# Kernel optimization log

Measured on AMD Instinct MI355X. Metric: run time of the kernel, lower is better.

Reference implementation:

```python
import jax, jax.numpy as jnp
import numpy as np

N = 100000
E = 1600000
F_IN = 512
HEADS = 8
C1 = 8          # per-head channels layer 1
C2 = 16         # num_classes, layer 2 (heads=1)
NEG_SLOPE = 0.2


def gat_conv(x, W, att_src, att_dst, bias, edge_index, heads, ch):
    """PyG-style GATConv (eval mode, add_self_loops=True, concat).
    x: [N, Fin], W: [Fin, heads*ch], att_*: [heads, ch], bias: [heads*ch]."""
    n = x.shape[0]
    loop = jnp.arange(n, dtype=edge_index.dtype)
    src = jnp.concatenate([edge_index[0], loop])   # [E+N]
    dst = jnp.concatenate([edge_index[1], loop])

    h = (x @ W).reshape(n, heads, ch)                       # [N, H, C]
    a_src = jnp.einsum('nhc,hc->nh', h, att_src)            # [N, H]
    a_dst = jnp.einsum('nhc,hc->nh', h, att_dst)

    e = a_src[src] + a_dst[dst]                             # [E+N, H]
    e = jax.nn.leaky_relu(e, NEG_SLOPE)
    # segment softmax over destination nodes
    m = jax.ops.segment_max(e, dst, num_segments=n)         # [N, H]
    ex = jnp.exp(e - m[dst])
    denom = jax.ops.segment_sum(ex, dst, num_segments=n)    # [N, H]
    alpha = ex / (denom[dst] + 1e-16)                       # [E+N, H]

    msg = h[src] * alpha[..., None]                         # [E+N, H, C]
    out = jax.ops.segment_sum(msg, dst, num_segments=n)     # [N, H, C]
    return out.reshape(n, heads * ch) + bias


def setup_inputs() -> dict:
    key = jax.random.key(0)
    ks = jax.random.split(key, 10)
    glorot = lambda k, shape: jax.random.normal(k, shape, jnp.float32) * np.sqrt(2.0 / (shape[0] + shape[-1]))
    return {
        'x': jax.random.normal(ks[0], (N, F_IN), jnp.float32),
        'edge_index': jax.random.randint(ks[1], (2, E), 0, N, jnp.int64),
        'W1': glorot(ks[2], (F_IN, HEADS * C1)),
        'att_src1': glorot(ks[3], (HEADS, C1)),
        'att_dst1': glorot(ks[4], (HEADS, C1)),
        'b1': jnp.zeros((HEADS * C1,), jnp.float32),
        'W2': glorot(ks[5], (HEADS * C1, C2)),
        'att_src2': glorot(ks[6], (1, C2)),
        'att_dst2': glorot(ks[7], (1, C2)),
        'b2': jnp.zeros((C2,), jnp.float32),
    }


def reference(x, edge_index, W1, att_src1, att_dst1, b1, W2, att_src2, att_dst2, b2):
    # eval mode: all F.dropout / internal attention dropout are identity
    h = gat_conv(x, W1, att_src1, att_dst1, b1, edge_index, HEADS, C1)   # [N, 64]
    h = jax.nn.elu(h)
    h = gat_conv(h, W2, att_src2, att_dst2, b2, edge_index, 1, C2)       # [N, C2]
    return jax.nn.log_softmax(h, axis=1)
```

## Files before the change

### kernel.cpp

```cpp
#include <hip/hip_runtime.h>
#include <hip/hip_bf16.h>

#define NEG_SLOPE 0.2f

typedef __attribute__((ext_vector_type(8))) short  bf16x8;
typedef __attribute__((ext_vector_type(8))) unsigned short u16x8;
typedef __attribute__((ext_vector_type(4))) unsigned short u16x4;
typedef __attribute__((ext_vector_type(4))) float  f32x4;

static __device__ __forceinline__ ushort f2bf(float f) {
    union { float f; unsigned int u; } c; c.f = f;
    unsigned int r = c.u + 0x7fffu + ((c.u >> 16) & 1u);
    return (ushort)(r >> 16);
}
static __device__ __forceinline__ float bf2f(ushort u) {
    union { unsigned int u; float f; } c; c.u = ((unsigned int)u) << 16;
    return c.f;
}

__global__ __launch_bounds__(256) void prep_w1(const float* __restrict__ W, ushort* __restrict__ W1T)
{
    int idx = blockIdx.x * 256 + threadIdx.x;
    if (idx >= 64 * 512) return;
    int c = idx >> 9, k = idx & 511;
    W1T[idx] = f2bf(W[k * 64 + c]);
}

__global__ __launch_bounds__(512, 4) void gemm1_mfma(
    const float* __restrict__ x, const ushort* __restrict__ W1T,
    const float* __restrict__ att_src, const float* __restrict__ att_dst,
    ushort* __restrict__ h1b, float* __restrict__ asrc, float* __restrict__ adst, int n)
{
    __shared__ ushort Bs[64][520];
    const int t    = threadIdx.x;
    const int lane = t & 63;
    const int wv   = t >> 6;
    const int rb   = blockIdx.x * 128;
    const int m    = lane & 15;
    const int kg   = lane >> 4;

    #pragma unroll
    for (int i = 0; i < 8; ++i) {
        int chunk = t + i * 512;
        int c  = chunk >> 6;
        int ko = (chunk & 63) * 8;
        *(u16x8*)&Bs[c][ko] = *(const u16x8*)(W1T + c * 512 + ko);
    }

    const int arow  = rb + wv * 16 + m;
    const int arowc = min(arow, n - 1);
    const float* xp = x + (size_t)arowc * 512 + kg * 8;

    f32x4 acc[4] = {};
    __syncthreads();

    float4 lo0 = *(const float4*)(xp);
    float4 hi0 = *(const float4*)(xp + 4);
    float4 lo1 = *(const float4*)(xp + 32);
    float4 hi1 = *(const float4*)(xp + 36);
    #pragma unroll
    for (int k32 = 0; k32 < 16; ++k32) {
        float4 nlo = {}, nhi = {};
        if (k32 < 14) {
            nlo = *(const float4*)(xp + (k32 + 2) * 32);
            nhi = *(const float4*)(xp + (k32 + 2) * 32 + 4);
        }
        u16x8 a;
        a[0] = f2bf(lo0.x); a[1] = f2bf(lo0.y); a[2] = f2bf(lo0.z); a[3] = f2bf(lo0.w);
        a[4] = f2bf(hi0.x); a[5] = f2bf(hi0.y); a[6] = f2bf(hi0.z); a[7] = f2bf(hi0.w);
        bf16x8 af = *(bf16x8*)&a;
        #pragma unroll
        for (int t4 = 0; t4 < 4; ++t4) {
            bf16x8 bfr = *(const bf16x8*)&Bs[t4 * 16 + m][k32 * 32 + kg * 8];
            acc[t4] = __builtin_amdgcn_mfma_f32_16x16x32_bf16(af, bfr, acc[t4], 0, 0, 0);
        }
        lo0 = lo1; hi0 = hi1; lo1 = nlo; hi1 = nhi;
    }

    #pragma unroll
    for (int t4 = 0; t4 < 4; ++t4) {
        const float as_w = att_src[t4 * 16 + m];
        const float ad_w = att_dst[t4 * 16 + m];
        #pragma unroll
        for (int i = 0; i < 4; ++i) {
            int gr = rb + wv * 16 + kg * 4 + i;
            float v = acc[t4][i];
            float ps = v * as_w, pd = v * ad_w;
            ps += __shfl_xor(ps, 1); pd += __shfl_xor(pd, 1);
            ps += __shfl_xor(ps, 2); pd += __shfl_xor(pd, 2);
            ps += __shfl_xor(ps, 4); pd += __shfl_xor(pd, 4);
            if (gr < n) {
                h1b[(size_t)gr * 64 + t4 * 16 + m] = f2bf(v);
                if ((m & 7) == 0) {
                    int h = t4 * 2 + (m >> 3);
                    asrc[gr * 8 + h] = ps;
                    adst[gr * 8 + h] = pd;
                }
            }
        }
    }
}

__global__ __launch_bounds__(256) void hist_k(
    const int* __restrict__ ei, int* __restrict__ cnt, int* __restrict__ slot, int E)
{
    int t = blockIdx.x * blockDim.x + threadIdx.x;
    if (t < E) slot[t] = atomicAdd(&cnt[ei[E + t]], 1);
}

#define SCAN_B 256
#define SCAN_T 256

__global__ __launch_bounds__(SCAN_T) void scan_a(const int* __restrict__ cnt, int* __restrict__ bsum, int n)
{
    __shared__ int sh[SCAN_T];
    const int tid = threadIdx.x;
    const int per = (n + SCAN_B * SCAN_T - 1) / (SCAN_B * SCAN_T);
    const int lo = (blockIdx.x * SCAN_T + tid) * per;
    const int hi = min(n, lo + per);
    int s = 0;
    for (int i = lo; i < hi; ++i) s += cnt[i];
    sh[tid] = s;
    __syncthreads();
    #pragma unroll
    for (int o = SCAN_T / 2; o; o >>= 1) {
        if (tid < o) sh[tid] += sh[tid + o];
        __syncthreads();
    }
    if (tid == 0) bsum[blockIdx.x] = sh[0];
}

__global__ __launch_bounds__(SCAN_T) void scan_b(
    const int* __restrict__ cnt, const int* __restrict__ bsum,
    int* __restrict__ rowptr, int n, int E)
{
    __shared__ int sb[SCAN_B];
    __shared__ int sh[SCAN_T];
    const int tid = threadIdx.x;
    sb[tid] = bsum[tid];
    __syncthreads();
    #pragma unroll
    for (int o = 1; o < SCAN_B; o <<= 1) {
        int v = (tid >= o) ? sb[tid - o] : 0;
        __syncthreads();
        sb[tid] += v;
        __syncthreads();
    }
    const int boff = (blockIdx.x == 0) ? 0 : sb[blockIdx.x - 1];

    const int per = (n + SCAN_B * SCAN_T - 1) / (SCAN_B * SCAN_T);
    const int lo = (blockIdx.x * SCAN_T + tid) * per;
    const int hi = min(n, lo + per);
    int s = 0;
    for (int i = lo; i < hi; ++i) s += cnt[i];
    sh[tid] = s;
    __syncthreads();
    #pragma unroll
    for (int o = 1; o < SCAN_T; o <<= 1) {
        int v = (tid >= o) ? sh[tid - o] : 0;
        __syncthreads();
        sh[tid] += v;
        __syncthreads();
    }
    int excl = boff + ((tid == 0) ? 0 : sh[tid - 1]);
    for (int i = lo; i < hi; ++i) { rowptr[i] = excl; excl += cnt[i]; }
    if (blockIdx.x == 0 && tid == 0) rowptr[n] = E;
}

__global__ __launch_bounds__(256) void scatter_k(
    const int* __restrict__ ei, const int* __restrict__ rowptr,
    const int* __restrict__ slot, int* __restrict__ ssrc, int E)
{
    int t = blockIdx.x * blockDim.x + threadIdx.x;
    if (t >= E) return;
    int d = ei[E + t];
    ssrc[rowptr[d] + slot[t]] = ei[t];
}

__global__ __launch_bounds__(256) void agg1_k(
    const int* __restrict__ rowptr, const int* __restrict__ ssrc,
    const float* __restrict__ asrc1, const float* __restrict__ adst1,
    const ushort* __restrict__ h1b, const float* __restrict__ b1,
    const float* __restrict__ W2, const float* __restrict__ att_src2, const float* __restrict__ att_dst2,
    ushort* __restrict__ h2b, float* __restrict__ asrc2, float* __restrict__ adst2, int n)
{
    __shared__ float Ws2[64 * 17];
    __shared__ float sv[4][64];
    const int t = threadIdx.x;
    #pragma unroll
    for (int k = 0; k < 4; ++k) {
        int idx = t + k * 256;
        Ws2[(idx >> 4) * 17 + (idx & 15)] = W2[idx];
    }
    __syncthreads();

    const int wv = t >> 6;
    const int j  = t & 63;
    const int g  = j >> 3;
    const int h  = j & 7;
    const int node = blockIdx.x * 4 + wv;
    const bool active = node < n;

    if (active) {
        const int d = node;
        const int start = rowptr[d], end = rowptr[d + 1];
        const float adsth = adst1[d * 8 + h];
        float acc0[8] = {}, acc1[8] = {};
        float dsum0 = 0.f, dsum1 = 0.f;
        for (int base = start - 1; base < end; base += 16) {
            int i0 = base + g;
            int i1 = i0 + 8;
            if (i0 < end) {
                int s = (i0 < start) ? d : ssrc[i0];
                float e = asrc1[s * 8 + h] + adsth;
                e = e > 0.f ? e : NEG_SLOPE * e;
                float ex = __expf(e);
                dsum0 += ex;
                u16x8 hv = *(const u16x8*)(h1b + (size_t)s * 64 + h * 8);
                #pragma unroll
                for (int c = 0; c < 8; ++c) acc0[c] += ex * bf2f(hv[c]);
            }
            if (i1 < end) {
                int s = ssrc[i1];
                float e = asrc1[s * 8 + h] + adsth;
                e = e > 0.f ? e : NEG_SLOPE * e;
                float ex = __expf(e);
                dsum1 += ex;
                u16x8 hv = *(const u16x8*)(h1b + (size_t)s * 64 + h * 8);
                #pragma unroll
                for (int c = 0; c < 8; ++c) acc1[c] += ex * bf2f(hv[c]);
            }
        }
        float dsum = dsum0 + dsum1;
        float acc[8];
        #pragma unroll
        for (int c = 0; c < 8; ++c) acc[c] = acc0[c] + acc1[c];
        #pragma unroll
        for (int o = 8; o < 64; o <<= 1) {
            dsum += __shfl_xor(dsum, o);
            #pragma unroll
            for (int c = 0; c < 8; ++c) acc[c] += __shfl_xor(acc[c], o);
        }
        if (g == 0) {
            float den = dsum + 1e-16f;
            #pragma unroll
            for (int c = 0; c < 8; ++c) {
                float v = acc[c] / den + b1[h * 8 + c];
                v = v > 0.f ? v : (__expf(v) - 1.f);
                sv[wv][h * 8 + c] = v;
            }
        }
    }
    __syncthreads();

    if (active) {
        const int c = j & 15, q = j >> 4;
        float p = 0.f;
        #pragma unroll
        for (int r = 0; r < 16; ++r)
            p += sv[wv][q * 16 + r] * Ws2[(q * 16 + r) * 17 + c];
        p += __shfl_xor(p, 16);
        p += __shfl_xor(p, 32);
        if (j < 16) h2b[(size_t)node * 16 + j] = f2bf(p);
        float as2 = p * att_src2[c];
        float ad2 = p * att_dst2[c];
        #pragma unroll
        for (int o = 1; o < 16; o <<= 1) { as2 += __shfl_xor(as2, o, 16); ad2 += __shfl_xor(ad2, o, 16); }
        if (j == 0) { asrc2[node] = as2; adst2[node] = ad2; }
    }
}

__global__ __launch_bounds__(256) void agg2_k(
    const int* __restrict__ rowptr, const int* __restrict__ ssrc,
    const float* __restrict__ asrc2, const float* __restrict__ adst2,
    const ushort* __restrict__ h2b, const float* __restrict__ b2,
    float* __restrict__ out, int n)
{
    const int t = threadIdx.x;
    const int node = blockIdx.x * 4 + (t >> 6);
    if (node >= n) return;
    const int j = t & 63;
    const int g = j >> 2;
    const int q = j & 3;
    const int d = node;
    const int start = rowptr[d], end = rowptr[d + 1];
    const float adst_d = adst2[d];

    float acc0[4] = {}, acc1[4] = {};
    float dsum0 = 0.f, dsum1 = 0.f;
    for (int base = start - 1; base < end; base += 32) {
        int i0 = base + g;
        int i1 = i0 + 16;
        if (i0 < end) {
            int s = (i0 < start) ? d : ssrc[i0];
            float e = asrc2[s] + adst_d;
            e = e > 0.f ? e : NEG_SLOPE * e;
            float ex = __expf(e);
            dsum0 += ex;
            u16x4 hv = *(const u16x4*)(h2b + (size_t)s * 16 + q * 4);
            #pragma unroll
            for (int c = 0; c < 4; ++c) acc0[c] += ex * bf2f(hv[c]);
        }
        if (i1 < end) {
            int s = ssrc[i1];
            float e = asrc2[s] + adst_d;
            e = e > 0.f ? e : NEG_SLOPE * e;
            float ex = __expf(e);
            dsum1 += ex;
            u16x4 hv = *(const u16x4*)(h2b + (size_t)s * 16 + q * 4);
            #pragma unroll
            for (int c = 0; c < 4; ++c) acc1[c] += ex * bf2f(hv[c]);
        }
    }
    float dsum = dsum0 + dsum1;
    float acc[4];
    #pragma unroll
    for (int c = 0; c < 4; ++c) acc[c] = acc0[c] + acc1[c];
    #pragma unroll
    for (int o = 4; o < 64; o <<= 1) {
        dsum += __shfl_xor(dsum, o);
        #pragma unroll
        for (int c = 0; c < 4; ++c) acc[c] += __shfl_xor(acc[c], o);
    }

    const float den = dsum + 1e-16f;
    float v[4];
    float m = -1e30f;
    #pragma unroll
    for (int c = 0; c < 4; ++c) {
        v[c] = acc[c] / den + b2[q * 4 + c];
        m = fmaxf(m, v[c]);
    }
    m = fmaxf(m, __shfl_xor(m, 1));
    m = fmaxf(m, __shfl_xor(m, 2));
    float s2 = 0.f;
    #pragma unroll
    for (int c = 0; c < 4; ++c) s2 += __expf(v[c] - m);
    s2 += __shfl_xor(s2, 1);
    s2 += __shfl_xor(s2, 2);
    const float lse = m + logf(s2);
    if (j < 4) {
        float4 o4 = make_float4(v[0] - lse, v[1] - lse, v[2] - lse, v[3] - lse);
        *(float4*)(out + (size_t)d * 16 + q * 4) = o4;
    }
}

static inline size_t align_up(size_t v, size_t a) { return (v + a - 1) & ~(a - 1); }

extern "C" void kernel_launch(void* const* d_in, const int* in_sizes, int n_in,
                              void* d_out, int out_size, void* d_ws, size_t ws_size,
                              hipStream_t stream) {
    const float* x        = (const float*)d_in[0];
    const int*   ei       = (const int*)d_in[1];
    const float* W1       = (const float*)d_in[2];
    const float* att_src1 = (const float*)d_in[3];
    const float* att_dst1 = (const float*)d_in[4];
    const float* b1       = (const float*)d_in[5];
    const float* W2       = (const float*)d_in[6];
    const float* att_src2 = (const float*)d_in[7];
    const float* att_dst2 = (const float*)d_in[8];
    const float* b2       = (const float*)d_in[9];
    float* out = (float*)d_out;

    const int n = in_sizes[0] / 512;
    const int E = in_sizes[1] / 2;

    char* base = (char*)d_ws;
    size_t off = 0;
    ushort* h1b   = (ushort*)(base + off); off = align_up(off + (size_t)128 * n, 64);
    ushort* h2b   = (ushort*)(base + off); off = align_up(off + (size_t)32 * n, 64);
    float*  asrc1 = (float*) (base + off); off = align_up(off + (size_t)32 * n, 64);
    float*  adst1 = (float*) (base + off); off = align_up(off + (size_t)32 * n, 64);
    float*  asrc2 = (float*) (base + off); off = align_up(off + (size_t)4 * n, 64);
    float*  adst2 = (float*) (base + off); off = align_up(off + (size_t)4 * n, 64);
    ushort* W1T   = (ushort*)(base + off); off = align_up(off + (size_t)65536, 64);
    int*    rowptr= (int*)   (base + off); off = align_up(off + (size_t)4 * (n + 1), 64);
    int*    cnt   = (int*)   (base + off); off = align_up(off + (size_t)4 * n, 64);
    int*    bsum  = (int*)   (base + off); off = align_up(off + (size_t)1024, 64);
    int*    slot  = (int*)   (base + off); off = align_up(off + (size_t)4 * E, 64);
    int*    ssrc  = (int*)   (base + off);

    hipMemsetAsync(cnt, 0, (size_t)4 * n, stream);

    prep_w1<<<128, 256, 0, stream>>>(W1, W1T);

    hist_k<<<(E + 255) / 256, 256, 0, stream>>>(ei, cnt, slot, E);
    scan_a<<<SCAN_B, SCAN_T, 0, stream>>>(cnt, bsum, n);
    scan_b<<<SCAN_B, SCAN_T, 0, stream>>>(cnt, bsum, rowptr, n, E);
    scatter_k<<<(E + 255) / 256, 256, 0, stream>>>(ei, rowptr, slot, ssrc, E);

    gemm1_mfma<<<(n + 127) / 128, 512, 0, stream>>>(x, W1T, att_src1, att_dst1, h1b, asrc1, adst1, n);

    agg1_k<<<(n + 3) / 4, 256, 0, stream>>>(rowptr, ssrc, asrc1, adst1, h1b, b1,
                                            W2, att_src2, att_dst2, h2b, asrc2, adst2, n);

    agg2_k<<<(n + 3) / 4, 256, 0, stream>>>(rowptr, ssrc, asrc2, adst2, h2b, b2, out, n);
}
```

Baseline: 269.3 us.

## Merge independent kernels via block-range dispatch and deepen x prefetch in GEMM

Combines W1 transpose/convert with the degree histogram into one launch, and the CSR scatter with the layer-1 GEMM into another, picking the role by block index so independent work shares a grid. This removes two kernel launches and lets the scatter and GEMM blocks run concurrently. The GEMM's register prefetch of x is also deepened from two to four k-steps ahead, raising register use. Scatter blocks now carry the GEMM's large static LDS allocation and the 512-thread, 4-wave-per-EU launch bounds, which may lower their occupancy.

```diff
diff --git a/kernel.cpp b/kernel.cpp
--- a/kernel.cpp
+++ b/kernel.cpp
@@ -18,24 +18,101 @@
     return c.f;
 }
 
-__global__ __launch_bounds__(256) void prep_w1(const float* __restrict__ W, ushort* __restrict__ W1T)
-{
-    int idx = blockIdx.x * 256 + threadIdx.x;
-    if (idx >= 64 * 512) return;
-    int c = idx >> 9, k = idx & 511;
-    W1T[idx] = f2bf(W[k * 64 + c]);
-}
-
-__global__ __launch_bounds__(512, 4) void gemm1_mfma(
+__global__ __launch_bounds__(256) void phase1_k(
+    const float* __restrict__ W, ushort* __restrict__ W1T,
+    const int* __restrict__ ei, int* __restrict__ cnt, int* __restrict__ slot, int E)
+{
+    if (blockIdx.x < 128) {
+        int idx = blockIdx.x * 256 + threadIdx.x;
+        int c = idx >> 9, k = idx & 511;
+        W1T[idx] = f2bf(W[k * 64 + c]);
+    } else {
+        int t = (blockIdx.x - 128) * 256 + threadIdx.x;
+        if (t < E) slot[t] = atomicAdd(&cnt[ei[E + t]], 1);
+    }
+}
+
+#define SCAN_B 256
+#define SCAN_T 256
+
+__global__ __launch_bounds__(SCAN_T) void scan_a(const int* __restrict__ cnt, int* __restrict__ bsum, int n)
+{
+    __shared__ int sh[SCAN_T];
+    const int tid = threadIdx.x;
+    const int per = (n + SCAN_B * SCAN_T - 1) / (SCAN_B * SCAN_T);
+    const int lo = (blockIdx.x * SCAN_T + tid) * per;
+    const int hi = min(n, lo + per);
+    int s = 0;
+    for (int i = lo; i < hi; ++i) s += cnt[i];
+    sh[tid] = s;
+    __syncthreads();
+    #pragma unroll
+    for (int o = SCAN_T / 2; o; o >>= 1) {
+        if (tid < o) sh[tid] += sh[tid + o];
+        __syncthreads();
+    }
+    if (tid == 0) bsum[blockIdx.x] = sh[0];
+}
+
+__global__ __launch_bounds__(SCAN_T) void scan_b(
+    const int* __restrict__ cnt, const int* __restrict__ bsum,
+    int* __restrict__ rowptr, int n, int E)
+{
+    __shared__ int sb[SCAN_B];
+    __shared__ int sh[SCAN_T];
+    const int tid = threadIdx.x;
+    sb[tid] = bsum[tid];
+    __syncthreads();
+    #pragma unroll
+    for (int o = 1; o < SCAN_B; o <<= 1) {
+        int v = (tid >= o) ? sb[tid - o] : 0;
+        __syncthreads();
+        sb[tid] += v;
+        __syncthreads();
+    }
+    const int boff = (blockIdx.x == 0) ? 0 : sb[blockIdx.x - 1];
+
+    const int per = (n + SCAN_B * SCAN_T - 1) / (SCAN_B * SCAN_T);
+    const int lo = (blockIdx.x * SCAN_T + tid) * per;
+    const int hi = min(n, lo + per);
+    int s = 0;
+    for (int i = lo; i < hi; ++i) s += cnt[i];
+    sh[tid] = s;
+    __syncthreads();
+    #pragma unroll
+    for (int o = 1; o < SCAN_T; o <<= 1) {
+        int v = (tid >= o) ? sh[tid - o] : 0;
+        __syncthreads();
+        sh[tid] += v;
+        __syncthreads();
+    }
+    int excl = boff + ((tid == 0) ? 0 : sh[tid - 1]);
+    for (int i = lo; i < hi; ++i) { rowptr[i] = excl; excl += cnt[i]; }
+    if (blockIdx.x == 0 && tid == 0) rowptr[n] = E;
+}
+
+__global__ __launch_bounds__(512, 4) void phase4_k(
+    const int* __restrict__ ei, const int* __restrict__ rowptr,
+    const int* __restrict__ slot, int* __restrict__ ssrc, int E, int Gs,
     const float* __restrict__ x, const ushort* __restrict__ W1T,
     const float* __restrict__ att_src, const float* __restrict__ att_dst,
     ushort* __restrict__ h1b, float* __restrict__ asrc, float* __restrict__ adst, int n)
 {
     __shared__ ushort Bs[64][520];
+
+    if ((int)blockIdx.x < Gs) {
+        int t = blockIdx.x * 512 + threadIdx.x;
+        if (t < E) {
+            int d = ei[E + t];
+            ssrc[rowptr[d] + slot[t]] = ei[t];
+        }
+        return;
+    }
+
     const int t    = threadIdx.x;
     const int lane = t & 63;
     const int wv   = t >> 6;
-    const int rb   = blockIdx.x * 128;
+    const int rb   = (blockIdx.x - Gs) * 128;
     const int m    = lane & 15;
     const int kg   = lane >> 4;
 
@@ -54,27 +131,28 @@
     f32x4 acc[4] = {};
     __syncthreads();
 
-    float4 lo0 = *(const float4*)(xp);
-    float4 hi0 = *(const float4*)(xp + 4);
-    float4 lo1 = *(const float4*)(xp + 32);
-    float4 hi1 = *(const float4*)(xp + 36);
+    float4 plo[4], phi[4];
+    #pragma unroll
+    for (int i = 0; i < 4; ++i) {
+        plo[i] = *(const float4*)(xp + i * 32);
+        phi[i] = *(const float4*)(xp + i * 32 + 4);
+    }
     #pragma unroll
     for (int k32 = 0; k32 < 16; ++k32) {
-        float4 nlo = {}, nhi = {};
-        if (k32 < 14) {
-            nlo = *(const float4*)(xp + (k32 + 2) * 32);
-            nhi = *(const float4*)(xp + (k32 + 2) * 32 + 4);
+        float4 lo = plo[k32 & 3], hi = phi[k32 & 3];
+        if (k32 + 4 < 16) {
+            plo[k32 & 3] = *(const float4*)(xp + (k32 + 4) * 32);
+            phi[k32 & 3] = *(const float4*)(xp + (k32 + 4) * 32 + 4);
         }
         u16x8 a;
-        a[0] = f2bf(lo0.x); a[1] = f2bf(lo0.y); a[2] = f2bf(lo0.z); a[3] = f2bf(lo0.w);
-        a[4] = f2bf(hi0.x); a[5] = f2bf(hi0.y); a[6] = f2bf(hi0.z); a[7] = f2bf(hi0.w);
+        a[0] = f2bf(lo.x); a[1] = f2bf(lo.y); a[2] = f2bf(lo.z); a[3] = f2bf(lo.w);
+        a[4] = f2bf(hi.x); a[5] = f2bf(hi.y); a[6] = f2bf(hi.z); a[7] = f2bf(hi.w);
         bf16x8 af = *(bf16x8*)&a;
         #pragma unroll
         for (int t4 = 0; t4 < 4; ++t4) {
             bf16x8 bfr = *(const bf16x8*)&Bs[t4 * 16 + m][k32 * 32 + kg * 8];
             acc[t4] = __builtin_amdgcn_mfma_f32_16x16x32_bf16(af, bfr, acc[t4], 0, 0, 0);
         }
-        lo0 = lo1; hi0 = hi1; lo1 = nlo; hi1 = nhi;
     }
 
     #pragma unroll
@@ -99,82 +177,6 @@
             }
         }
     }
-}
-
-__global__ __launch_bounds__(256) void hist_k(
-    const int* __restrict__ ei, int* __restrict__ cnt, int* __restrict__ slot, int E)
-{
-    int t = blockIdx.x * blockDim.x + threadIdx.x;
-    if (t < E) slot[t] = atomicAdd(&cnt[ei[E + t]], 1);
-}
-
-#define SCAN_B 256
-#define SCAN_T 256
-
-__global__ __launch_bounds__(SCAN_T) void scan_a(const int* __restrict__ cnt, int* __restrict__ bsum, int n)
-{
-    __shared__ int sh[SCAN_T];
-    const int tid = threadIdx.x;
-    const int per = (n + SCAN_B * SCAN_T - 1) / (SCAN_B * SCAN_T);
-    const int lo = (blockIdx.x * SCAN_T + tid) * per;
-    const int hi = min(n, lo + per);
-    int s = 0;
-    for (int i = lo; i < hi; ++i) s += cnt[i];
-    sh[tid] = s;
-    __syncthreads();
-    #pragma unroll
-    for (int o = SCAN_T / 2; o; o >>= 1) {
-        if (tid < o) sh[tid] += sh[tid + o];
-        __syncthreads();
-    }
-    if (tid == 0) bsum[blockIdx.x] = sh[0];
-}
-
-__global__ __launch_bounds__(SCAN_T) void scan_b(
-    const int* __restrict__ cnt, const int* __restrict__ bsum,
-    int* __restrict__ rowptr, int n, int E)
-{
-    __shared__ int sb[SCAN_B];
-    __shared__ int sh[SCAN_T];
-    const int tid = threadIdx.x;
-    sb[tid] = bsum[tid];
-    __syncthreads();
-    #pragma unroll
-    for (int o = 1; o < SCAN_B; o <<= 1) {
-        int v = (tid >= o) ? sb[tid - o] : 0;
-        __syncthreads();
-        sb[tid] += v;
-        __syncthreads();
-    }
-    const int boff = (blockIdx.x == 0) ? 0 : sb[blockIdx.x - 1];
-
-    const int per = (n + SCAN_B * SCAN_T - 1) / (SCAN_B * SCAN_T);
-    const int lo = (blockIdx.x * SCAN_T + tid) * per;
-    const int hi = min(n, lo + per);
-    int s = 0;
-    for (int i = lo; i < hi; ++i) s += cnt[i];
-    sh[tid] = s;
-    __syncthreads();
-    #pragma unroll
-    for (int o = 1; o < SCAN_T; o <<= 1) {
-        int v = (tid >= o) ? sh[tid - o] : 0;
-        __syncthreads();
-        sh[tid] += v;
-        __syncthreads();
-    }
-    int excl = boff + ((tid == 0) ? 0 : sh[tid - 1]);
-    for (int i = lo; i < hi; ++i) { rowptr[i] = excl; excl += cnt[i]; }
-    if (blockIdx.x == 0 && tid == 0) rowptr[n] = E;
-}
-
-__global__ __launch_bounds__(256) void scatter_k(
-    const int* __restrict__ ei, const int* __restrict__ rowptr,
-    const int* __restrict__ slot, int* __restrict__ ssrc, int E)
-{
-    int t = blockIdx.x * blockDim.x + threadIdx.x;
-    if (t >= E) return;
-    int d = ei[E + t];
-    ssrc[rowptr[d] + slot[t]] = ei[t];
 }
 
 __global__ __launch_bounds__(256) void agg1_k(
@@ -382,14 +384,15 @@
 
     hipMemsetAsync(cnt, 0, (size_t)4 * n, stream);
 
-    prep_w1<<<128, 256, 0, stream>>>(W1, W1T);
-
-    hist_k<<<(E + 255) / 256, 256, 0, stream>>>(ei, cnt, slot, E);
+    phase1_k<<<128 + (E + 255) / 256, 256, 0, stream>>>(W1, W1T, ei, cnt, slot, E);
+
     scan_a<<<SCAN_B, SCAN_T, 0, stream>>>(cnt, bsum, n);
     scan_b<<<SCAN_B, SCAN_T, 0, stream>>>(cnt, bsum, rowptr, n, E);
-    scatter_k<<<(E + 255) / 256, 256, 0, stream>>>(ei, rowptr, slot, ssrc, E);
-
-    gemm1_mfma<<<(n + 127) / 128, 512, 0, stream>>>(x, W1T, att_src1, att_dst1, h1b, asrc1, adst1, n);
+
+    const int Gs = (E + 511) / 512;
+    const int Gg = (n + 127) / 128;
+    phase4_k<<<Gs + Gg, 512, 0, stream>>>(ei, rowptr, slot, ssrc, E, Gs,
+                                          x, W1T, att_src1, att_dst1, h1b, asrc1, adst1, n);
 
     agg1_k<<<(n + 3) / 4, 256, 0, stream>>>(rowptr, ssrc, asrc1, adst1, h1b, b1,
                                             W2, att_src2, att_dst2, h2b, asrc2, adst2, n);
```

Measured after the change: 268.5 us. No clear change (-0.3%).
